# Kernel optimization log

Measured on AMD Instinct MI355X. Metric: run time of the kernel, lower is better.

The kernel has to match this reference:

```python
import jax, jax.numpy as jnp
import numpy as np

N_NODES = 100000
N_EDGES = 1000000
IN_DIM = 128
HID1 = 64
HID2 = 64
OUT_DIM = 1
NUM_GRAPHS = 2048


def setup_inputs() -> dict:
    key = jax.random.key(0)
    ks = jax.random.split(key, 12)
    x = jax.random.normal(ks[0], (N_NODES, IN_DIM), dtype=jnp.float32)
    edge_index = jax.random.randint(ks[1], (2, N_EDGES), 0, N_NODES, dtype=jnp.int64)
    batch = jnp.sort(jax.random.randint(ks[2], (N_NODES,), 0, NUM_GRAPHS, dtype=jnp.int64))
    s1 = 1.0 / np.sqrt(IN_DIM)
    s2 = 1.0 / np.sqrt(HID1)
    s3 = 1.0 / np.sqrt(HID2)
    return {
        "x": x,
        "edge_index": edge_index,
        "batch": batch,
        "W1": jax.random.normal(ks[3], (IN_DIM, HID1), dtype=jnp.float32) * s1,
        "b1": jnp.zeros((HID1,), dtype=jnp.float32),
        "W2": jax.random.normal(ks[4], (HID1, HID2), dtype=jnp.float32) * s2,
        "b2": jnp.zeros((HID2,), dtype=jnp.float32),
        "attn_w": jax.random.normal(ks[5], (HID2, 1), dtype=jnp.float32) * s3,
        "attn_b": jnp.zeros((1,), dtype=jnp.float32),
        "mask_w": jax.random.normal(ks[6], (HID2, 1), dtype=jnp.float32) * s3,
        "mask_b": jnp.zeros((1,), dtype=jnp.float32),
        "out_w": jax.random.normal(ks[7], (HID2, OUT_DIM), dtype=jnp.float32) * s3,
        "out_b": jnp.zeros((OUT_DIM,), dtype=jnp.float32),
    }


def reference(x, edge_index, batch, W1, b1, W2, b2, attn_w, attn_b, mask_w, mask_b, out_w, out_b):
    n = x.shape[0]
    # GCNConv (PyG default): add self-loops, symmetric normalization
    loop = jnp.arange(n, dtype=edge_index.dtype)
    row = jnp.concatenate([edge_index[0], loop])  # source nodes
    col = jnp.concatenate([edge_index[1], loop])  # target nodes
    deg = jax.ops.segment_sum(jnp.ones_like(col, dtype=x.dtype), col, num_segments=n)
    dinv = jnp.where(deg > 0, jax.lax.rsqrt(jnp.maximum(deg, 1e-12)), 0.0)
    norm = dinv[row] * dinv[col]  # [E+N]

    def conv(h, W, b):
        h = h @ W                              # [N, out]
        m = h[row] * norm[:, None]             # gather + scale  [E+N, out]
        return jax.ops.segment_sum(m, col, num_segments=n) + b

    h = jax.nn.relu(conv(x, W1, b1))
    h = jax.nn.relu(conv(h, W2, b2))
    # AttentionPooling: (attn score * sigmoid mask)-weighted scatter-sum per graph
    scores = (h @ attn_w + attn_b) * jax.nn.sigmoid(h @ mask_w + mask_b)  # [N,1]
    pooled = jax.ops.segment_sum(h * scores, batch, num_segments=NUM_GRAPHS)  # [G, HID2]
    return pooled @ out_w + out_b
```

## Files before the change

kernel.cpp:

```cpp
#include <hip/hip_runtime.h>
#include <hip/hip_fp16.h>
#include <math.h>


#define NB 64
#define SEG 16
#define CAPS 80
#define SLOTS (SEG * CAPS)
#define BIN_BLOCKS 256

__device__ __forceinline__ void h8_set(float* a, const int4 w) {
    const __half2* h = (const __half2*)&w;
    float2 t0 = __half22float2(h[0]);
    float2 t1 = __half22float2(h[1]);
    float2 t2 = __half22float2(h[2]);
    float2 t3 = __half22float2(h[3]);
    a[0] = t0.x; a[1] = t0.y; a[2] = t1.x; a[3] = t1.y;
    a[4] = t2.x; a[5] = t2.y; a[6] = t3.x; a[7] = t3.y;
}
__device__ __forceinline__ void h8_acc(float* a, const int4 w) {
    const __half2* h = (const __half2*)&w;
    float2 t0 = __half22float2(h[0]);
    float2 t1 = __half22float2(h[1]);
    float2 t2 = __half22float2(h[2]);
    float2 t3 = __half22float2(h[3]);
    a[0] += t0.x; a[1] += t0.y; a[2] += t1.x; a[3] += t1.y;
    a[4] += t2.x; a[5] += t2.y; a[6] += t3.x; a[7] += t3.y;
}

__global__ __launch_bounds__(256) void gemm_bin_kernel(
    const float* __restrict__ X, const float* __restrict__ W,
    __half* __restrict__ P, int N, int K,
    const int* __restrict__ row, const int* __restrict__ col,
    int* __restrict__ bcnt, int* __restrict__ gbuf, int E,
    float* __restrict__ out, const float* __restrict__ out_b, int G) {
    __shared__ float Wl[32 * 64];
    __shared__ float xs[32 * 132];

    if (blockIdx.x < BIN_BLOCKS) {
        int seg = blockIdx.x & (SEG - 1);
        int t = blockIdx.x * 256 + threadIdx.x;
        if (t < G) out[t] = out_b[0];
        for (int e = t; e < E; e += BIN_BLOCKS * 256) {
            int c = col[e];
            int b = c >> 6;
            int pos = atomicAdd(&bcnt[(b * SEG + seg) * 16], 1);
            if (pos < CAPS) gbuf[b * SLOTS + seg * CAPS + pos] = row[e] | ((c & 63) << 17);
        }
        return;
    }

    const int tid = threadIdx.x;
    const int cg = tid & 7;
    const int ng = tid >> 3;
    const int node0 = (blockIdx.x - BIN_BLOCKS) * 128;

    float acc[4][8];
#pragma unroll
    for (int r = 0; r < 4; r++)
#pragma unroll
        for (int j = 0; j < 8; j++) acc[r][j] = 0.0f;

    for (int k0 = 0; k0 < K; k0 += 32) {
        const float4* Wg = (const float4*)(W + (size_t)k0 * 64);
#pragma unroll
        for (int f = tid; f < 512; f += 256) ((float4*)Wl)[f] = Wg[f];
        {
            int rrow = tid >> 1;
            int q0 = (tid & 1) * 16;
            int node = node0 + rrow;
            const float* Xr = X + (size_t)node * K + k0 + q0;
#pragma unroll
            for (int q = 0; q < 4; q++) {
                float4 v = make_float4(0.f, 0.f, 0.f, 0.f);
                if (node < N) v = *(const float4*)(Xr + 4 * q);
                int kb = q0 + 4 * q;
                xs[(kb + 0) * 132 + rrow] = v.x;
                xs[(kb + 1) * 132 + rrow] = v.y;
                xs[(kb + 2) * 132 + rrow] = v.z;
                xs[(kb + 3) * 132 + rrow] = v.w;
            }
        }
        __syncthreads();
#pragma unroll
        for (int kk = 0; kk < 32; kk++) {
            float4 xv = *(const float4*)&xs[kk * 132 + ng * 4];
            const float* wr = &Wl[kk * 64 + cg * 8];
            float4 w0 = *(const float4*)(wr + 0);
            float4 w1 = *(const float4*)(wr + 4);
#pragma unroll
            for (int r = 0; r < 4; r++) {
                float xr = (r == 0) ? xv.x : (r == 1) ? xv.y : (r == 2) ? xv.z : xv.w;
                acc[r][0] = fmaf(xr, w0.x, acc[r][0]);
                acc[r][1] = fmaf(xr, w0.y, acc[r][1]);
                acc[r][2] = fmaf(xr, w0.z, acc[r][2]);
                acc[r][3] = fmaf(xr, w0.w, acc[r][3]);
                acc[r][4] = fmaf(xr, w1.x, acc[r][4]);
                acc[r][5] = fmaf(xr, w1.y, acc[r][5]);
                acc[r][6] = fmaf(xr, w1.z, acc[r][6]);
                acc[r][7] = fmaf(xr, w1.w, acc[r][7]);
            }
        }
        __syncthreads();
    }

#pragma unroll
    for (int r = 0; r < 4; r++) {
        int node = node0 + ng * 4 + r;
        if (node < N) {
            __half2 hh[4];
            hh[0] = __floats2half2_rn(acc[r][0], acc[r][1]);
            hh[1] = __floats2half2_rn(acc[r][2], acc[r][3]);
            hh[2] = __floats2half2_rn(acc[r][4], acc[r][5]);
            hh[3] = __floats2half2_rn(acc[r][6], acc[r][7]);
            ((int4*)(P + (size_t)node * 64))[cg] = *(int4*)hh;
        }
    }
}

__global__ __launch_bounds__(256) void sort_kernel(
    const int* __restrict__ bcnt, const int* __restrict__ gbuf,
    int* __restrict__ csr, int* __restrict__ startcnt,
    float* __restrict__ dinv, __half* __restrict__ P, int N) {
    __shared__ int scnt[SEG], segoff[SEG], s_tot;
    __shared__ int ebuf[SLOTS];
    __shared__ int lcnt[NB], lcur[NB];
    __shared__ float sdinv[NB];
    const int tid = threadIdx.x;
    const int b = blockIdx.x;
    const int base = b * SLOTS;

    if (tid < SEG) {
        int c = bcnt[(b * SEG + tid) * 16];
        scnt[tid] = c < CAPS ? c : CAPS;
    }
    if (tid < NB) lcnt[tid] = 0;
    __syncthreads();
    if (tid == 0) {
        int o = 0;
        for (int s = 0; s < SEG; s++) { segoff[s] = o; o += scnt[s]; }
        s_tot = o;
    }
    __syncthreads();
    for (int idx = tid; idx < SLOTS; idx += 256) {
        int seg = idx / CAPS;
        int j = idx - seg * CAPS;
        if (j < scnt[seg]) {
            int w = gbuf[base + idx];
            ebuf[segoff[seg] + j] = w;
            atomicAdd(&lcnt[(w >> 17) & 63], 1);
        }
    }
    __syncthreads();
    if (tid < NB) {
        int cntv = lcnt[tid];
        int rnd = (cntv + 3) & ~3;
        int val = rnd;
#pragma unroll
        for (int off = 1; off < 64; off <<= 1) {
            int n = __shfl_up(val, off, 64);
            if (tid >= off) val += n;
        }
        int st = val - rnd;
        lcur[tid] = st;
        float d = rsqrtf(1.0f + (float)cntv);
        sdinv[tid] = d;
        int v = b * NB + tid;
        if (v < N) {
            dinv[v] = d;
            int cc = cntv < 127 ? cntv : 127;
            startcnt[v] = ((base + st) << 7) | cc;
        }
    }
    __syncthreads();
    int tot = s_tot;
    for (int idx = tid; idx < tot; idx += 256) {
        int w = ebuf[idx];
        int vl = (w >> 17) & 63;
        int pp = atomicAdd(&lcur[vl], 1);
        csr[base + pp] = w & 131071;
    }
    for (int idx = tid; idx < NB * 8; idx += 256) {
        int r = idx >> 3;
        int v = b * NB + r;
        if (v < N) {
            float d = sdinv[r];
            int4* pp = (int4*)(P + (size_t)v * 64) + (idx & 7);
            int4 t = *pp;
            __half2* hp = (__half2*)&t;
#pragma unroll
            for (int q = 0; q < 4; q++) {
                float2 f = __half22float2(hp[q]);
                hp[q] = __floats2half2_rn(f.x * d, f.y * d);
            }
            *pp = t;
        }
    }
}

__global__ __launch_bounds__(256) void gather_gemm_kernel(
    const __half* __restrict__ P, const int* __restrict__ csr,
    const int* __restrict__ startcnt, const float* __restrict__ dinv,
    const float* __restrict__ b1, const float* __restrict__ W2,
    __half* __restrict__ Q, int N) {
    __shared__ float hs[64 * 65];
    const int tid = threadIdx.x;
    const int v0 = blockIdx.x * 64;
    const int vend = (v0 + 64 < N) ? v0 + 64 : N;
    const int p = tid & 7;

    const float4 bb0 = ((const float4*)b1)[2 * p];
    const float4 bb1 = ((const float4*)b1)[2 * p + 1];
    for (int v = v0 + (tid >> 3); v < vend; v += 32) {
        int pack = startcnt[v];
        int st = pack >> 7;
        int c = pack & 127;
        float dv = dinv[v];
        float a[8];
        h8_set(a, ((const int4*)(P + (size_t)v * 64))[p]);
        for (int i = 0; i < c; i += 8) {
            int4 ua = *(const int4*)(csr + st + i);
            int4 ub = *(const int4*)(csr + st + i + 4);
            int4 m0 = ((const int4*)(P + (size_t)ua.x * 64))[p];
            int4 m1 = ((const int4*)(P + (size_t)ua.y * 64))[p];
            int4 m2 = ((const int4*)(P + (size_t)ua.z * 64))[p];
            int4 m3 = ((const int4*)(P + (size_t)ua.w * 64))[p];
            int4 m4 = ((const int4*)(P + (size_t)ub.x * 64))[p];
            int4 m5 = ((const int4*)(P + (size_t)ub.y * 64))[p];
            int4 m6 = ((const int4*)(P + (size_t)ub.z * 64))[p];
            int4 m7 = ((const int4*)(P + (size_t)ub.w * 64))[p];
            h8_acc(a, m0);
            if (i + 1 < c) h8_acc(a, m1);
            if (i + 2 < c) h8_acc(a, m2);
            if (i + 3 < c) h8_acc(a, m3);
            if (i + 4 < c) h8_acc(a, m4);
            if (i + 5 < c) h8_acc(a, m5);
            if (i + 6 < c) h8_acc(a, m6);
            if (i + 7 < c) h8_acc(a, m7);
        }
        float* hd = &hs[(v - v0) * 65 + p * 8];
        hd[0] = fmaxf(fmaf(a[0], dv, bb0.x), 0.f);
        hd[1] = fmaxf(fmaf(a[1], dv, bb0.y), 0.f);
        hd[2] = fmaxf(fmaf(a[2], dv, bb0.z), 0.f);
        hd[3] = fmaxf(fmaf(a[3], dv, bb0.w), 0.f);
        hd[4] = fmaxf(fmaf(a[4], dv, bb1.x), 0.f);
        hd[5] = fmaxf(fmaf(a[5], dv, bb1.y), 0.f);
        hd[6] = fmaxf(fmaf(a[6], dv, bb1.z), 0.f);
        hd[7] = fmaxf(fmaf(a[7], dv, bb1.w), 0.f);
    }
    __syncthreads();

    const int cg = tid & 7;
    const int n0 = tid >> 3;
    float acc2[2][8];
#pragma unroll
    for (int r = 0; r < 2; r++)
#pragma unroll
        for (int j = 0; j < 8; j++) acc2[r][j] = 0.0f;
    for (int kk = 0; kk < 64; kk++) {
        float x0 = hs[(n0 * 2 + 0) * 65 + kk];
        float x1 = hs[(n0 * 2 + 1) * 65 + kk];
        const float* wr = W2 + kk * 64 + cg * 8;
        float4 w0 = *(const float4*)(wr + 0);
        float4 w1 = *(const float4*)(wr + 4);
        acc2[0][0] = fmaf(x0, w0.x, acc2[0][0]);
        acc2[0][1] = fmaf(x0, w0.y, acc2[0][1]);
        acc2[0][2] = fmaf(x0, w0.z, acc2[0][2]);
        acc2[0][3] = fmaf(x0, w0.w, acc2[0][3]);
        acc2[0][4] = fmaf(x0, w1.x, acc2[0][4]);
        acc2[0][5] = fmaf(x0, w1.y, acc2[0][5]);
        acc2[0][6] = fmaf(x0, w1.z, acc2[0][6]);
        acc2[0][7] = fmaf(x0, w1.w, acc2[0][7]);
        acc2[1][0] = fmaf(x1, w0.x, acc2[1][0]);
        acc2[1][1] = fmaf(x1, w0.y, acc2[1][1]);
        acc2[1][2] = fmaf(x1, w0.z, acc2[1][2]);
        acc2[1][3] = fmaf(x1, w0.w, acc2[1][3]);
        acc2[1][4] = fmaf(x1, w1.x, acc2[1][4]);
        acc2[1][5] = fmaf(x1, w1.y, acc2[1][5]);
        acc2[1][6] = fmaf(x1, w1.z, acc2[1][6]);
        acc2[1][7] = fmaf(x1, w1.w, acc2[1][7]);
    }
#pragma unroll
    for (int r = 0; r < 2; r++) {
        int node = v0 + n0 * 2 + r;
        if (node < N) {
            float d = dinv[node];
            __half2 hh[4];
            hh[0] = __floats2half2_rn(acc2[r][0] * d, acc2[r][1] * d);
            hh[1] = __floats2half2_rn(acc2[r][2] * d, acc2[r][3] * d);
            hh[2] = __floats2half2_rn(acc2[r][4] * d, acc2[r][5] * d);
            hh[3] = __floats2half2_rn(acc2[r][6] * d, acc2[r][7] * d);
            ((int4*)(Q + (size_t)node * 64))[cg] = *(int4*)hh;
        }
    }
}

#define GP_NODES 64
__global__ __launch_bounds__(256) void gather_pool_kernel(
    const __half* __restrict__ Q, const int* __restrict__ csr,
    const int* __restrict__ startcnt, const float* __restrict__ dinv,
    const float* __restrict__ bias, const int* __restrict__ batch,
    const float* __restrict__ attn_w, const float* __restrict__ attn_b,
    const float* __restrict__ mask_w, const float* __restrict__ mask_b,
    const float* __restrict__ out_w, float* __restrict__ out, int N) {
    __shared__ float pacc[2048];
    __shared__ int s_gmin, s_span;
    const int tid = threadIdx.x;
    const int v0 = blockIdx.x * GP_NODES;
    const int vend = (v0 + GP_NODES < N) ? v0 + GP_NODES : N;
    if (tid == 0) {
        int gmin = batch[v0];
        s_gmin = gmin;
        s_span = batch[vend - 1] - gmin + 1;
    }
    __syncthreads();
    const int gmin = s_gmin, span = s_span;
    for (int i = tid; i < span; i += 256) pacc[i] = 0.f;
    __syncthreads();

    const int p = tid & 7;
    const float4 wa0 = ((const float4*)attn_w)[2 * p], wa1 = ((const float4*)attn_w)[2 * p + 1];
    const float4 wm0 = ((const float4*)mask_w)[2 * p], wm1 = ((const float4*)mask_w)[2 * p + 1];
    const float4 wo0 = ((const float4*)out_w)[2 * p],  wo1 = ((const float4*)out_w)[2 * p + 1];
    const float4 bb0 = ((const float4*)bias)[2 * p],   bb1 = ((const float4*)bias)[2 * p + 1];
    const float ab = attn_b[0], mb = mask_b[0];

    for (int v = v0 + (tid >> 3); v < vend; v += 32) {
        int pack = startcnt[v];
        int st = pack >> 7;
        int c = pack & 127;
        float dv = dinv[v];
        float a[8];
        h8_set(a, ((const int4*)(Q + (size_t)v * 64))[p]);
        for (int i = 0; i < c; i += 8) {
            int4 ua = *(const int4*)(csr + st + i);
            int4 ub = *(const int4*)(csr + st + i + 4);
            int4 m0 = ((const int4*)(Q + (size_t)ua.x * 64))[p];
            int4 m1 = ((const int4*)(Q + (size_t)ua.y * 64))[p];
            int4 m2 = ((const int4*)(Q + (size_t)ua.z * 64))[p];
            int4 m3 = ((const int4*)(Q + (size_t)ua.w * 64))[p];
            int4 m4 = ((const int4*)(Q + (size_t)ub.x * 64))[p];
            int4 m5 = ((const int4*)(Q + (size_t)ub.y * 64))[p];
            int4 m6 = ((const int4*)(Q + (size_t)ub.z * 64))[p];
            int4 m7 = ((const int4*)(Q + (size_t)ub.w * 64))[p];
            h8_acc(a, m0);
            if (i + 1 < c) h8_acc(a, m1);
            if (i + 2 < c) h8_acc(a, m2);
            if (i + 3 < c) h8_acc(a, m3);
            if (i + 4 < c) h8_acc(a, m4);
            if (i + 5 < c) h8_acc(a, m5);
            if (i + 6 < c) h8_acc(a, m6);
            if (i + 7 < c) h8_acc(a, m7);
        }
        float h0 = fmaxf(fmaf(a[0], dv, bb0.x), 0.f);
        float h1v = fmaxf(fmaf(a[1], dv, bb0.y), 0.f);
        float h2v = fmaxf(fmaf(a[2], dv, bb0.z), 0.f);
        float h3 = fmaxf(fmaf(a[3], dv, bb0.w), 0.f);
        float h4 = fmaxf(fmaf(a[4], dv, bb1.x), 0.f);
        float h5 = fmaxf(fmaf(a[5], dv, bb1.y), 0.f);
        float h6 = fmaxf(fmaf(a[6], dv, bb1.z), 0.f);
        float h7 = fmaxf(fmaf(a[7], dv, bb1.w), 0.f);
        float pa = h0 * wa0.x + h1v * wa0.y + h2v * wa0.z + h3 * wa0.w
                 + h4 * wa1.x + h5 * wa1.y + h6 * wa1.z + h7 * wa1.w;
        float pm = h0 * wm0.x + h1v * wm0.y + h2v * wm0.z + h3 * wm0.w
                 + h4 * wm1.x + h5 * wm1.y + h6 * wm1.z + h7 * wm1.w;
        float po = h0 * wo0.x + h1v * wo0.y + h2v * wo0.z + h3 * wo0.w
                 + h4 * wo1.x + h5 * wo1.y + h6 * wo1.z + h7 * wo1.w;
#pragma unroll
        for (int off = 1; off < 8; off <<= 1) {
            pa += __shfl_xor(pa, off, 64);
            pm += __shfl_xor(pm, off, 64);
            po += __shfl_xor(po, off, 64);
        }
        if (p == 0) {
            float cc = (pa + ab) * (1.0f / (1.0f + expf(-(pm + mb)))) * po;
            atomicAdd(&pacc[batch[v] - gmin], cc);
        }
    }
    __syncthreads();
    for (int i = tid; i < span; i += 256) {
        float val = pacc[i];
        if (val != 0.f) atomicAdd(&out[gmin + i], val);
    }
}

extern "C" void kernel_launch(void* const* d_in, const int* in_sizes, int n_in,
                              void* d_out, int out_size, void* d_ws, size_t ws_size,
                              hipStream_t stream) {
    const float* x      = (const float*)d_in[0];
    const int*   edge   = (const int*)d_in[1];
    const int*   batch  = (const int*)d_in[2];
    const float* W1     = (const float*)d_in[3];
    const float* b1     = (const float*)d_in[4];
    const float* W2     = (const float*)d_in[5];
    const float* b2     = (const float*)d_in[6];
    const float* attn_w = (const float*)d_in[7];
    const float* attn_b = (const float*)d_in[8];
    const float* mask_w = (const float*)d_in[9];
    const float* mask_b = (const float*)d_in[10];
    const float* out_w  = (const float*)d_in[11];
    const float* out_b  = (const float*)d_in[12];
    float* out = (float*)d_out;

    const int N  = in_sizes[2];
    const int E  = in_sizes[1] / 2;
    const int K1 = in_sizes[0] / N;
    const int H  = in_sizes[4];
    const int G  = out_size;
    const int* row = edge;
    const int* col = edge + E;

    const int NBUCK = (N + NB - 1) / NB;

    char* ws = (char*)d_ws;
    auto align256 = [](size_t s) { return (s + 255) / 256 * 256; };
    int*    bcnt     = (int*)ws;    ws += align256((size_t)NBUCK * SEG * 16 * 4);
    int*    gbuf     = (int*)ws;    ws += align256((size_t)NBUCK * SLOTS * 4);
    int*    csr      = (int*)ws;    ws += align256((size_t)NBUCK * SLOTS * 4);
    int*    startcnt = (int*)ws;    ws += align256((size_t)N * 4);
    float*  dinv     = (float*)ws;  ws += align256((size_t)N * 4);
    __half* P        = (__half*)ws; ws += align256((size_t)N * H * 2);
    __half* Q        = (__half*)ws;

    const int gblocks = (N + 127) / 128;

    hipMemsetAsync(bcnt, 0, (size_t)NBUCK * SEG * 16 * 4, stream);
    hipMemsetAsync(csr, 0, (size_t)NBUCK * SLOTS * 4, stream);

    gemm_bin_kernel<<<BIN_BLOCKS + gblocks, 256, 0, stream>>>(
        x, W1, P, N, K1, row, col, bcnt, gbuf, E, out, out_b, G);

    sort_kernel<<<NBUCK, 256, 0, stream>>>(bcnt, gbuf, csr, startcnt, dinv, P, N);

    gather_gemm_kernel<<<NBUCK, 256, 0, stream>>>(
        P, csr, startcnt, dinv, b1, W2, Q, N);

    gather_pool_kernel<<<NBUCK, 256, 0, stream>>>(
        Q, csr, startcnt, dinv, b2, batch, attn_w, attn_b, mask_w, mask_b, out_w, out, N);
}
```

Before: 237.7 us.

## Store Q in feature-sliced layout and gather slice-by-slice in pooling kernel

The second-layer activations Q are now written as 8 separate feature slices (16 bytes per node each) instead of one 128-byte row per node. The pooling kernel gathers one slice at a time, with 4 threads per node splitting the neighbor list, then combines with shuffles and stages the result in shared memory before the attention/pool step. The aim is a smaller working set per pass so gathers hit cache better, at the cost of 8 passes over the CSR indices and scalar index loads. W2 is also staged into shared memory for the GEMM.

```diff
diff --git a/kernel.cpp b/kernel.cpp
--- a/kernel.cpp
+++ b/kernel.cpp
@@ -204,10 +204,14 @@
     const float* __restrict__ b1, const float* __restrict__ W2,
     __half* __restrict__ Q, int N) {
     __shared__ float hs[64 * 65];
+    __shared__ float Wl[64 * 64];
     const int tid = threadIdx.x;
     const int v0 = blockIdx.x * 64;
     const int vend = (v0 + 64 < N) ? v0 + 64 : N;
     const int p = tid & 7;
+
+    for (int f = tid; f < 1024; f += 256)
+        ((float4*)Wl)[f] = ((const float4*)W2)[f];
 
     const float4 bb0 = ((const float4*)b1)[2 * p];
     const float4 bb1 = ((const float4*)b1)[2 * p + 1];
@@ -260,7 +264,7 @@
     for (int kk = 0; kk < 64; kk++) {
         float x0 = hs[(n0 * 2 + 0) * 65 + kk];
         float x1 = hs[(n0 * 2 + 1) * 65 + kk];
-        const float* wr = W2 + kk * 64 + cg * 8;
+        const float* wr = &Wl[kk * 64 + cg * 8];
         float4 w0 = *(const float4*)(wr + 0);
         float4 w1 = *(const float4*)(wr + 4);
         acc2[0][0] = fmaf(x0, w0.x, acc2[0][0]);
@@ -290,7 +294,7 @@
             hh[1] = __floats2half2_rn(acc2[r][2] * d, acc2[r][3] * d);
             hh[2] = __floats2half2_rn(acc2[r][4] * d, acc2[r][5] * d);
             hh[3] = __floats2half2_rn(acc2[r][6] * d, acc2[r][7] * d);
-            ((int4*)(Q + (size_t)node * 64))[cg] = *(int4*)hh;
+            *(int4*)(Q + (size_t)cg * N * 8 + (size_t)node * 8) = *(int4*)hh;
         }
     }
 }
@@ -303,6 +307,7 @@
     const float* __restrict__ attn_w, const float* __restrict__ attn_b,
     const float* __restrict__ mask_w, const float* __restrict__ mask_b,
     const float* __restrict__ out_w, float* __restrict__ out, int N) {
+    __shared__ float h2s[64 * 65];
     __shared__ float pacc[2048];
     __shared__ int s_gmin, s_span;
     const int tid = threadIdx.x;
@@ -316,50 +321,61 @@
     __syncthreads();
     const int gmin = s_gmin, span = s_span;
     for (int i = tid; i < span; i += 256) pacc[i] = 0.f;
+
+    const int vi = tid >> 2;
+    const int j = tid & 3;
+    const int v = v0 + vi;
+    const bool alive = v < N;
+    int st = 0, c = 0;
+    float dv = 0.f;
+    if (alive) {
+        int pack = startcnt[v];
+        st = pack >> 7;
+        c = pack & 127;
+        dv = dinv[v];
+    }
+    for (int s = 0; s < 8; s++) {
+        const __half* Qs = Q + (size_t)s * N * 8;
+        float a[8] = {0.f, 0.f, 0.f, 0.f, 0.f, 0.f, 0.f, 0.f};
+        if (alive) {
+            if (j == 0) h8_acc(a, *(const int4*)(Qs + (size_t)v * 8));
+            for (int i = j; i < c; i += 4) {
+                int u = csr[st + i];
+                h8_acc(a, *(const int4*)(Qs + (size_t)u * 8));
+            }
+        }
+#pragma unroll
+        for (int k = 0; k < 8; k++) {
+            a[k] += __shfl_xor(a[k], 1, 64);
+            a[k] += __shfl_xor(a[k], 2, 64);
+        }
+        if (alive && j == 0) {
+            float4 bb0 = ((const float4*)bias)[2 * s];
+            float4 bb1 = ((const float4*)bias)[2 * s + 1];
+            float* hd = &h2s[vi * 65 + s * 8];
+            hd[0] = fmaxf(fmaf(a[0], dv, bb0.x), 0.f);
+            hd[1] = fmaxf(fmaf(a[1], dv, bb0.y), 0.f);
+            hd[2] = fmaxf(fmaf(a[2], dv, bb0.z), 0.f);
+            hd[3] = fmaxf(fmaf(a[3], dv, bb0.w), 0.f);
+            hd[4] = fmaxf(fmaf(a[4], dv, bb1.x), 0.f);
+            hd[5] = fmaxf(fmaf(a[5], dv, bb1.y), 0.f);
+            hd[6] = fmaxf(fmaf(a[6], dv, bb1.z), 0.f);
+            hd[7] = fmaxf(fmaf(a[7], dv, bb1.w), 0.f);
+        }
+    }
     __syncthreads();
 
     const int p = tid & 7;
+    const int g = tid >> 3;
     const float4 wa0 = ((const float4*)attn_w)[2 * p], wa1 = ((const float4*)attn_w)[2 * p + 1];
     const float4 wm0 = ((const float4*)mask_w)[2 * p], wm1 = ((const float4*)mask_w)[2 * p + 1];
     const float4 wo0 = ((const float4*)out_w)[2 * p],  wo1 = ((const float4*)out_w)[2 * p + 1];
-    const float4 bb0 = ((const float4*)bias)[2 * p],   bb1 = ((const float4*)bias)[2 * p + 1];
     const float ab = attn_b[0], mb = mask_b[0];
 
-    for (int v = v0 + (tid >> 3); v < vend; v += 32) {
-        int pack = startcnt[v];
-        int st = pack >> 7;
-        int c = pack & 127;
-        float dv = dinv[v];
-        float a[8];
-        h8_set(a, ((const int4*)(Q + (size_t)v * 64))[p]);
-        for (int i = 0; i < c; i += 8) {
-            int4 ua = *(const int4*)(csr + st + i);
-            int4 ub = *(const int4*)(csr + st + i + 4);
-            int4 m0 = ((const int4*)(Q + (size_t)ua.x * 64))[p];
-            int4 m1 = ((const int4*)(Q + (size_t)ua.y * 64))[p];
-            int4 m2 = ((const int4*)(Q + (size_t)ua.z * 64))[p];
-            int4 m3 = ((const int4*)(Q + (size_t)ua.w * 64))[p];
-            int4 m4 = ((const int4*)(Q + (size_t)ub.x * 64))[p];
-            int4 m5 = ((const int4*)(Q + (size_t)ub.y * 64))[p];
-            int4 m6 = ((const int4*)(Q + (size_t)ub.z * 64))[p];
-            int4 m7 = ((const int4*)(Q + (size_t)ub.w * 64))[p];
-            h8_acc(a, m0);
-            if (i + 1 < c) h8_acc(a, m1);
-            if (i + 2 < c) h8_acc(a, m2);
-            if (i + 3 < c) h8_acc(a, m3);
-            if (i + 4 < c) h8_acc(a, m4);
-            if (i + 5 < c) h8_acc(a, m5);
-            if (i + 6 < c) h8_acc(a, m6);
-            if (i + 7 < c) h8_acc(a, m7);
-        }
-        float h0 = fmaxf(fmaf(a[0], dv, bb0.x), 0.f);
-        float h1v = fmaxf(fmaf(a[1], dv, bb0.y), 0.f);
-        float h2v = fmaxf(fmaf(a[2], dv, bb0.z), 0.f);
-        float h3 = fmaxf(fmaf(a[3], dv, bb0.w), 0.f);
-        float h4 = fmaxf(fmaf(a[4], dv, bb1.x), 0.f);
-        float h5 = fmaxf(fmaf(a[5], dv, bb1.y), 0.f);
-        float h6 = fmaxf(fmaf(a[6], dv, bb1.z), 0.f);
-        float h7 = fmaxf(fmaf(a[7], dv, bb1.w), 0.f);
+    for (int vv = g; vv < GP_NODES; vv += 32) {
+        const float* hd = &h2s[vv * 65 + p * 8];
+        float h0 = hd[0], h1v = hd[1], h2v = hd[2], h3 = hd[3];
+        float h4 = hd[4], h5 = hd[5], h6 = hd[6], h7 = hd[7];
         float pa = h0 * wa0.x + h1v * wa0.y + h2v * wa0.z + h3 * wa0.w
                  + h4 * wa1.x + h5 * wa1.y + h6 * wa1.z + h7 * wa1.w;
         float pm = h0 * wm0.x + h1v * wm0.y + h2v * wm0.z + h3 * wm0.w
@@ -372,9 +388,10 @@
             pm += __shfl_xor(pm, off, 64);
             po += __shfl_xor(po, off, 64);
         }
-        if (p == 0) {
+        int node = v0 + vv;
+        if (p == 0 && node < N) {
             float cc = (pa + ab) * (1.0f / (1.0f + expf(-(pm + mb)))) * po;
-            atomicAdd(&pacc[batch[v] - gmin], cc);
+            atomicAdd(&pacc[batch[node] - gmin], cc);
         }
     }
     __syncthreads();
```

Result: slower. 275.1 us (+15.8%).
